# Performance work log

Hardware: AMD Instinct MI355X
Metric: run time of the kernel (lower is better)

The kernel has to match this reference:

```python
import jax, jax.numpy as jnp
import numpy as np
from functools import partial

HID = 16
EMB = 32

def setup_inputs() -> dict:
    key = jax.random.key(0)
    ks = jax.random.split(key, 9)
    S, B, V = 64, 32, 50257
    stdv = 1.0 / np.sqrt(HID)
    u = lambda k, shp: jax.random.uniform(k, shp, jnp.float32, -stdv, stdv)
    return {
        "input_batch": jax.random.randint(ks[0], (S, B), 0, V),
        "embedding": u(ks[1], (V, EMB)),  # original re-inits randn embedding with uniform via init_params
        "W_lr": u(ks[2], (HID, EMB + HID)),
        "b_lr": u(ks[3], (HID,)),
        "W_rl": u(ks[4], (HID, EMB + HID)),
        "b_rl": u(ks[5], (HID,)),
        "W_ho": u(ks[6], (V, 2 * HID)),
        "b_ho": u(ks[7], (V,)),
        "h0": u(ks[8], (1, HID)),
    }


def _rnn_pre_states(emb, W, b, h0):
    # emb: [S,B,E]; returns stacked hidden states BEFORE each step: [S,B,H]
    def step(h, x):
        h_new = jnp.tanh(jnp.concatenate([x, h], axis=-1) @ W.T + b)
        return h_new, h  # collect pre-update state
    _, pre = jax.lax.scan(step, h0, emb)
    return pre


def reference(input_batch, embedding, W_lr, b_lr, W_rl, b_rl, W_ho, b_ho, h0):
    S, B = input_batch.shape
    emb = embedding[input_batch]                      # [S,B,EMB]
    h0b = jnp.broadcast_to(h0, (B, HID))
    # Left-to-right: prediction at i uses hLR state before consuming word i
    hLR_pre = _rnn_pre_states(emb, W_lr, b_lr, h0b)   # [S,B,HID]
    # Right-to-left: run over reversed sequence, collect pre-states, reverse back
    hRL_pre = _rnn_pre_states(emb[::-1], W_rl, b_rl, h0b)[::-1]  # [S,B,HID]
    h = jnp.concatenate([hLR_pre, hRL_pre], axis=-1)  # [S,B,2*HID]
    logits = jnp.einsum('sbh,vh->sbv', h, W_ho) + b_ho
    return jax.nn.log_softmax(logits, axis=-1)        # [S,B,V]
```

## Files before the change

kernel.cpp:

```cpp
#include <hip/hip_runtime.h>
#include <hip/hip_bf16.h>

#define S 64
#define B 32
#define HID 16
#define EMB 32
#define V 50257
#define NCB 197
#define VP4 51200
#define M 2048
#define PREP_BLOCKS (VP4*EMB/256)
#define NRG 4
#define RT_PER (128/NRG)
#define CPG 25

using bf16x8 = __attribute__((ext_vector_type(8))) __bf16;
using f32x4  = __attribute__((ext_vector_type(4))) float;

__global__ void k_prep(const float* __restrict__ W_ho, const float* __restrict__ b_ho,
                       const int* __restrict__ idx, const float* __restrict__ emb,
                       const float* __restrict__ W_lr, const float* __restrict__ b_lr,
                       const float* __restrict__ W_rl, const float* __restrict__ b_rl,
                       __bf16* __restrict__ Wb, float* __restrict__ bias,
                       float* __restrict__ P) {
    const int bx = blockIdx.x;
    if (bx < PREP_BLOCKS) {
        int i = bx * 256 + threadIdx.x;
        if (i < VP4) bias[i] = (i < V) ? b_ho[i] : -1e30f;
        int v = i >> 5;
        Wb[i] = (v < V) ? (__bf16)W_ho[i] : (__bf16)0.f;
    } else {
        int i = (bx - PREP_BLOCKS) * 256 + threadIdx.x;
        const int dir = i >> 15, r = i & 32767, m = r >> 4, j = r & 15;
        const float* W  = dir ? W_rl : W_lr;
        const float* bb = dir ? b_rl : b_lr;
        const int tok = idx[m];
        const float4* er = reinterpret_cast<const float4*>(emb + (size_t)tok * EMB);
        const float4* wr = reinterpret_cast<const float4*>(W + j * (EMB + HID));
        float acc = bb[j];
        #pragma unroll
        for (int q = 0; q < 8; ++q) {
            float4 e4 = er[q], w4 = wr[q];
            acc += e4.x * w4.x + e4.y * w4.y + e4.z * w4.z + e4.w * w4.w;
        }
        P[i] = acc;
    }
}

__global__ void k_rnn(const float* __restrict__ P,
                      const float* __restrict__ W_lr, const float* __restrict__ W_rl,
                      const float* __restrict__ h0, __bf16* __restrict__ hcat) {
    __shared__ float Psh[S * 4 * HID];
    __shared__ float hsh[4][17];
    const int t = threadIdx.x;
    const int dir = blockIdx.x >> 3, bq = blockIdx.x & 7;
    const int bl = t >> 4, j = t & 15;
    const int b = bq * 4 + bl;
    {
        const float4* Pg4 = reinterpret_cast<const float4*>(P);
        float4* Ps4 = reinterpret_cast<float4*>(Psh);
        #pragma unroll
        for (int i = 0; i < 16; ++i) {
            int s = (t >> 4) + 4 * i;
            Ps4[t + 64 * i] = Pg4[dir * 8192 + s * 128 + bq * 16 + (t & 15)];
        }
    }
    const float* Wd = (dir ? W_rl : W_lr) + j * (EMB + HID) + EMB;
    float wh[16];
    #pragma unroll
    for (int q = 0; q < 4; ++q) {
        float4 w4 = *reinterpret_cast<const float4*>(Wd + q * 4);
        wh[q * 4 + 0] = w4.x; wh[q * 4 + 1] = w4.y;
        wh[q * 4 + 2] = w4.z; wh[q * 4 + 3] = w4.w;
    }
    float hcur = h0[j];
    hsh[bl][j] = hcur;
    for (int step = 0; step < S; ++step) {
        const int s = dir ? (S - 1 - step) : step;
        hcat[(s * B + b) * 32 + dir * HID + j] = (__bf16)hcur;
        float acc = Psh[s * 64 + bl * 16 + j];
        #pragma unroll
        for (int k = 0; k < HID; ++k) acc += wh[k] * hsh[bl][k];
        hcur = tanhf(acc);
        hsh[bl][j] = hcur;
    }
}

__global__ void k_pass1(const __bf16* __restrict__ hb, const __bf16* __restrict__ Wb,
                        const float* __restrict__ bias, float* __restrict__ partials) {
    const int cbx = blockIdx.x, rg = blockIdx.y;
    const int wave = threadIdx.x >> 6, lane = threadIdx.x & 63;
    const int lr = lane & 15, kg = lane >> 4;
    const int ttbase = cbx * 16 + wave * 4;
    bf16x8 wfrag[4]; float bc[4];
    #pragma unroll
    for (int q = 0; q < 4; ++q) {
        wfrag[q] = *reinterpret_cast<const bf16x8*>(Wb + ((ttbase + q) * 16 + lr) * 32 + kg * 8);
        bc[q] = bias[(ttbase + q) * 16 + lr];
    }
    __shared__ float red[4][16];
    const f32x4 zero = {0.f, 0.f, 0.f, 0.f};
    for (int rt = rg * RT_PER; rt < rg * RT_PER + RT_PER; ++rt) {
        const int m0 = rt * 16;
        const bf16x8 a = *reinterpret_cast<const bf16x8*>(hb + (m0 + lr) * 32 + kg * 8);
        float s0 = 0.f, s1 = 0.f, s2 = 0.f, s3 = 0.f;
        #pragma unroll
        for (int q = 0; q < 4; ++q) {
            f32x4 d = __builtin_amdgcn_mfma_f32_16x16x32_bf16(a, wfrag[q], zero, 0, 0, 0);
            s0 += __expf(d[0] + bc[q]);
            s1 += __expf(d[1] + bc[q]);
            s2 += __expf(d[2] + bc[q]);
            s3 += __expf(d[3] + bc[q]);
        }
        #pragma unroll
        for (int off = 1; off < 16; off <<= 1) {
            s0 += __shfl_xor(s0, off);
            s1 += __shfl_xor(s1, off);
            s2 += __shfl_xor(s2, off);
            s3 += __shfl_xor(s3, off);
        }
        if (lr == 0) {
            red[wave][kg * 4 + 0] = s0;
            red[wave][kg * 4 + 1] = s1;
            red[wave][kg * 4 + 2] = s2;
            red[wave][kg * 4 + 3] = s3;
        }
        __syncthreads();
        if (threadIdx.x < 16)
            partials[cbx * M + m0 + threadIdx.x] =
                red[0][threadIdx.x] + red[1][threadIdx.x] +
                red[2][threadIdx.x] + red[3][threadIdx.x];
        __syncthreads();
    }
}

__device__ __forceinline__ void p2_load(const __bf16* __restrict__ Wb,
                                        const float* __restrict__ bias,
                                        int chunk, int wave, int lr, int kg,
                                        bf16x8* wf, float* bc) {
    const int t0 = chunk * 16 + wave * 4;
    #pragma unroll
    for (int q = 0; q < 4; ++q) {
        wf[q] = *reinterpret_cast<const bf16x8*>(Wb + ((t0 + q) * 16 + lr) * 32 + kg * 8);
        bc[q] = bias[(t0 + q) * 16 + lr];
    }
}

template <bool GUARD>
__device__ __forceinline__ void p2_cs(const bf16x8* wf, const float* bc, bf16x8 a,
                                      const float* lzr, int chunk, int wave,
                                      int lane, int lr, int kg, int m0,
                                      float* __restrict__ out, float (*st)[68]) {
    const f32x4 zero = {0.f, 0.f, 0.f, 0.f};
    #pragma unroll
    for (int q = 0; q < 4; ++q) {
        f32x4 d = __builtin_amdgcn_mfma_f32_16x16x32_bf16(a, wf[q], zero, 0, 0, 0);
        const int cl = q * 16 + lr;
        #pragma unroll
        for (int r = 0; r < 4; ++r)
            st[kg * 4 + r][cl] = d[r] + bc[q] - lzr[r];
    }
    asm volatile("s_waitcnt lgkmcnt(0)" ::: "memory");
    __builtin_amdgcn_sched_barrier(0);
    const int cb0 = chunk * 256 + wave * 64;
    const int vcol = cb0 + lane;
    float* p = out + (size_t)m0 * V + vcol;
    #pragma unroll
    for (int r = 0; r < 16; ++r) {
        if (!GUARD || vcol < V)
            p[(size_t)r * V] = st[r][lane];
    }
}

__global__ __launch_bounds__(256, 4) void k_pass2(
        const __bf16* __restrict__ hb, const __bf16* __restrict__ Wb,
        const float* __restrict__ bias, const float* __restrict__ partials,
        float* __restrict__ out) {
    __shared__ float red[16][17];
    __shared__ float lzsh[16];
    __shared__ float stg[2][4][16][68];
    const int cg = blockIdx.x, rt = blockIdx.y;
    const int t = threadIdx.x;
    const int m0 = rt * 16;
    {
        const int row = t & 15, cch = t >> 4;
        float p = 0.f;
        for (int c = cch; c < NCB; c += 16) p += partials[c * M + m0 + row];
        red[cch][row] = p;
        __syncthreads();
        if (t < 16) {
            float tot = 0.f;
            #pragma unroll
            for (int k = 0; k < 16; ++k) tot += red[k][t];
            lzsh[t] = __logf(tot);
        }
        __syncthreads();
    }
    const int wave = t >> 6, lane = t & 63;
    const int lr = lane & 15, kg = lane >> 4;
    const bf16x8 a = *reinterpret_cast<const bf16x8*>(hb + (m0 + lr) * 32 + kg * 8);
    float lzr[4];
    #pragma unroll
    for (int r = 0; r < 4; ++r) lzr[r] = lzsh[kg * 4 + r];
    float (*stA)[68] = stg[0][wave];
    float (*stB)[68] = stg[1][wave];
    const int c0 = cg * CPG;

    bf16x8 wfA[4], wfB[4];
    float bcA[4], bcB[4];
    p2_load(Wb, bias, c0, wave, lr, kg, wfA, bcA);
    if (cg < 7) {
        for (int g = 0; g < 12; ++g) {
            p2_load(Wb, bias, c0 + 2 * g + 1, wave, lr, kg, wfB, bcB);
            p2_cs<false>(wfA, bcA, a, lzr, c0 + 2 * g, wave, lane, lr, kg, m0, out, stA);
            p2_load(Wb, bias, c0 + 2 * g + 2, wave, lr, kg, wfA, bcA);
            p2_cs<false>(wfB, bcB, a, lzr, c0 + 2 * g + 1, wave, lane, lr, kg, m0, out, stB);
        }
        p2_cs<false>(wfA, bcA, a, lzr, c0 + 24, wave, lane, lr, kg, m0, out, stA);
    } else {
        for (int g = 0; g < 12; ++g) {
            p2_load(Wb, bias, c0 + 2 * g + 1, wave, lr, kg, wfB, bcB);
            p2_cs<true>(wfA, bcA, a, lzr, c0 + 2 * g, wave, lane, lr, kg, m0, out, stA);
            p2_load(Wb, bias, c0 + 2 * g + 2, wave, lr, kg, wfA, bcA);
            p2_cs<true>(wfB, bcB, a, lzr, c0 + 2 * g + 1, wave, lane, lr, kg, m0, out, stB);
        }
        p2_cs<true>(wfA, bcA, a, lzr, c0 + 24, wave, lane, lr, kg, m0, out, stA);
    }
}

extern "C" void kernel_launch(void* const* d_in, const int* in_sizes, int n_in,
                              void* d_out, int out_size, void* d_ws, size_t ws_size,
                              hipStream_t stream) {
    const int*   idx       = (const int*)d_in[0];
    const float* embedding = (const float*)d_in[1];
    const float* W_lr      = (const float*)d_in[2];
    const float* b_lr      = (const float*)d_in[3];
    const float* W_rl      = (const float*)d_in[4];
    const float* b_rl      = (const float*)d_in[5];
    const float* W_ho      = (const float*)d_in[6];
    const float* b_ho      = (const float*)d_in[7];
    const float* h0        = (const float*)d_in[8];
    float* out = (float*)d_out;

    char* ws = (char*)d_ws;
    size_t off = 0;
    __bf16* Wb      = (__bf16*)(ws + off); off += (size_t)VP4 * EMB * 2;
    float*  bias    = (float*)(ws + off);  off += (size_t)VP4 * 4;
    __bf16* hb      = (__bf16*)(ws + off); off += (size_t)M * 32 * 2;
    float*  P       = (float*)(ws + off);  off += (size_t)2 * M * HID * 4;
    float*  partials= (float*)(ws + off);  off += (size_t)NCB * M * 4;

    k_prep<<<PREP_BLOCKS + 256, 256, 0, stream>>>(W_ho, b_ho, idx, embedding,
                                                  W_lr, b_lr, W_rl, b_rl, Wb, bias, P);
    k_rnn<<<16, 64, 0, stream>>>(P, W_lr, W_rl, h0, hb);
    k_pass1<<<dim3(NCB, NRG), 256, 0, stream>>>(hb, Wb, bias, partials);
    k_pass2<<<dim3(8, 128), 256, 0, stream>>>(hb, Wb, bias, partials, out);
}
```

Measured before the change: 186.2 us.

## Fuse all stages into one cooperative persistent kernel with grid syncs

Replaces the four separate launches (prep, RNN, pass1 partial sums, pass2 write) with a single cooperative kernel of 512 blocks that uses grid-wide syncs between phases. The bf16 weight conversion now runs in parallel with the serial RNN on the otherwise idle blocks, and the logsumexp partials are reduced over 8 column groups instead of 197. Each block handles two row tiles. This removes launch gaps and hides the RNN latency, at the cost of three grid barriers, lower occupancy (launch bounds 2) and a longer serial per-block loop in pass1.

After: 445.4 us. 139% more time.

```diff
diff --git a/kernel.cpp b/kernel.cpp
--- a/kernel.cpp
+++ b/kernel.cpp
@@ -1,36 +1,85 @@
 #include <hip/hip_runtime.h>
 #include <hip/hip_bf16.h>
+#include <hip/hip_cooperative_groups.h>
 
 #define S 64
 #define B 32
 #define HID 16
 #define EMB 32
 #define V 50257
-#define NCB 197
 #define VP4 51200
 #define M 2048
-#define PREP_BLOCKS (VP4*EMB/256)
-#define NRG 4
-#define RT_PER (128/NRG)
+#define NCG 8
+#define TPW 100
 #define CPG 25
+#define WB_STRIDE (496*256)
+
+namespace cgrp = cooperative_groups;
 
 using bf16x8 = __attribute__((ext_vector_type(8))) __bf16;
 using f32x4  = __attribute__((ext_vector_type(4))) float;
 
-__global__ void k_prep(const float* __restrict__ W_ho, const float* __restrict__ b_ho,
-                       const int* __restrict__ idx, const float* __restrict__ emb,
-                       const float* __restrict__ W_lr, const float* __restrict__ b_lr,
-                       const float* __restrict__ W_rl, const float* __restrict__ b_rl,
-                       __bf16* __restrict__ Wb, float* __restrict__ bias,
-                       float* __restrict__ P) {
-    const int bx = blockIdx.x;
-    if (bx < PREP_BLOCKS) {
-        int i = bx * 256 + threadIdx.x;
-        if (i < VP4) bias[i] = (i < V) ? b_ho[i] : -1e30f;
-        int v = i >> 5;
-        Wb[i] = (v < V) ? (__bf16)W_ho[i] : (__bf16)0.f;
-    } else {
-        int i = (bx - PREP_BLOCKS) * 256 + threadIdx.x;
+__device__ __forceinline__ void p2_load(const __bf16* __restrict__ Wb,
+                                        const float* __restrict__ bias,
+                                        int chunk, int wave, int lr, int kg,
+                                        bf16x8* wf, float* bc) {
+    const int t0 = chunk * 16 + wave * 4;
+    #pragma unroll
+    for (int q = 0; q < 4; ++q) {
+        wf[q] = *reinterpret_cast<const bf16x8*>(Wb + ((t0 + q) * 16 + lr) * 32 + kg * 8);
+        bc[q] = bias[(t0 + q) * 16 + lr];
+    }
+}
+
+template <bool GUARD>
+__device__ __forceinline__ void p2_cs(const bf16x8* wf, const float* bc, bf16x8 a,
+                                      const float* lzr, int chunk, int wave,
+                                      int lane, int lr, int kg, int m0,
+                                      float* __restrict__ out, float (*st)[68]) {
+    const f32x4 zero = {0.f, 0.f, 0.f, 0.f};
+    #pragma unroll
+    for (int q = 0; q < 4; ++q) {
+        f32x4 d = __builtin_amdgcn_mfma_f32_16x16x32_bf16(a, wf[q], zero, 0, 0, 0);
+        const int cl = q * 16 + lr;
+        #pragma unroll
+        for (int r = 0; r < 4; ++r)
+            st[kg * 4 + r][cl] = d[r] + bc[q] - lzr[r];
+    }
+    asm volatile("s_waitcnt lgkmcnt(0)" ::: "memory");
+    __builtin_amdgcn_sched_barrier(0);
+    const int cb0 = chunk * 256 + wave * 64;
+    const int vcol = cb0 + lane;
+    float* p = out + (size_t)m0 * V + vcol;
+    #pragma unroll
+    for (int r = 0; r < 16; ++r) {
+        if (!GUARD || vcol < V)
+            p[(size_t)r * V] = st[r][lane];
+    }
+}
+
+__global__ __launch_bounds__(256, 2) void k_all(
+        const int* __restrict__ idx, const float* __restrict__ emb,
+        const float* __restrict__ W_lr, const float* __restrict__ b_lr,
+        const float* __restrict__ W_rl, const float* __restrict__ b_rl,
+        const float* __restrict__ W_ho, const float* __restrict__ b_ho,
+        const float* __restrict__ h0,
+        __bf16* __restrict__ Wb, float* __restrict__ bias,
+        __bf16* __restrict__ hb, float* __restrict__ P,
+        float* __restrict__ Zp, float* __restrict__ out) {
+    __shared__ float Psh[S * 4 * HID];
+    __shared__ float hsh[4][17];
+    __shared__ float red[2][4][16];
+    __shared__ float lzsh[2][16];
+    __shared__ float stg[2][4][16][68];
+
+    const int cg = blockIdx.x, ry = blockIdx.y;
+    const int bid = cg + NCG * ry;
+    const int t = threadIdx.x;
+    const int gtid = bid * 256 + t;
+
+    if (gtid < VP4) bias[gtid] = (gtid < V) ? b_ho[gtid] : -1e30f;
+    if (gtid < 2 * M * HID) {
+        const int i = gtid;
         const int dir = i >> 15, r = i & 32767, m = r >> 4, j = r & 15;
         const float* W  = dir ? W_rl : W_lr;
         const float* bb = dir ? b_rl : b_lr;
@@ -45,186 +94,125 @@
         }
         P[i] = acc;
     }
-}
-
-__global__ void k_rnn(const float* __restrict__ P,
-                      const float* __restrict__ W_lr, const float* __restrict__ W_rl,
-                      const float* __restrict__ h0, __bf16* __restrict__ hcat) {
-    __shared__ float Psh[S * 4 * HID];
-    __shared__ float hsh[4][17];
-    const int t = threadIdx.x;
-    const int dir = blockIdx.x >> 3, bq = blockIdx.x & 7;
-    const int bl = t >> 4, j = t & 15;
-    const int b = bq * 4 + bl;
-    {
-        const float4* Pg4 = reinterpret_cast<const float4*>(P);
-        float4* Ps4 = reinterpret_cast<float4*>(Psh);
-        #pragma unroll
-        for (int i = 0; i < 16; ++i) {
-            int s = (t >> 4) + 4 * i;
-            Ps4[t + 64 * i] = Pg4[dir * 8192 + s * 128 + bq * 16 + (t & 15)];
-        }
-    }
-    const float* Wd = (dir ? W_rl : W_lr) + j * (EMB + HID) + EMB;
-    float wh[16];
-    #pragma unroll
-    for (int q = 0; q < 4; ++q) {
-        float4 w4 = *reinterpret_cast<const float4*>(Wd + q * 4);
-        wh[q * 4 + 0] = w4.x; wh[q * 4 + 1] = w4.y;
-        wh[q * 4 + 2] = w4.z; wh[q * 4 + 3] = w4.w;
-    }
-    float hcur = h0[j];
-    hsh[bl][j] = hcur;
-    for (int step = 0; step < S; ++step) {
-        const int s = dir ? (S - 1 - step) : step;
-        hcat[(s * B + b) * 32 + dir * HID + j] = (__bf16)hcur;
-        float acc = Psh[s * 64 + bl * 16 + j];
-        #pragma unroll
-        for (int k = 0; k < HID; ++k) acc += wh[k] * hsh[bl][k];
-        hcur = tanhf(acc);
-        hsh[bl][j] = hcur;
-    }
-}
-
-__global__ void k_pass1(const __bf16* __restrict__ hb, const __bf16* __restrict__ Wb,
-                        const float* __restrict__ bias, float* __restrict__ partials) {
-    const int cbx = blockIdx.x, rg = blockIdx.y;
-    const int wave = threadIdx.x >> 6, lane = threadIdx.x & 63;
-    const int lr = lane & 15, kg = lane >> 4;
-    const int ttbase = cbx * 16 + wave * 4;
-    bf16x8 wfrag[4]; float bc[4];
-    #pragma unroll
-    for (int q = 0; q < 4; ++q) {
-        wfrag[q] = *reinterpret_cast<const bf16x8*>(Wb + ((ttbase + q) * 16 + lr) * 32 + kg * 8);
-        bc[q] = bias[(ttbase + q) * 16 + lr];
-    }
-    __shared__ float red[4][16];
-    const f32x4 zero = {0.f, 0.f, 0.f, 0.f};
-    for (int rt = rg * RT_PER; rt < rg * RT_PER + RT_PER; ++rt) {
-        const int m0 = rt * 16;
-        const bf16x8 a = *reinterpret_cast<const bf16x8*>(hb + (m0 + lr) * 32 + kg * 8);
-        float s0 = 0.f, s1 = 0.f, s2 = 0.f, s3 = 0.f;
-        #pragma unroll
-        for (int q = 0; q < 4; ++q) {
-            f32x4 d = __builtin_amdgcn_mfma_f32_16x16x32_bf16(a, wfrag[q], zero, 0, 0, 0);
-            s0 += __expf(d[0] + bc[q]);
-            s1 += __expf(d[1] + bc[q]);
-            s2 += __expf(d[2] + bc[q]);
-            s3 += __expf(d[3] + bc[q]);
-        }
-        #pragma unroll
-        for (int off = 1; off < 16; off <<= 1) {
-            s0 += __shfl_xor(s0, off);
-            s1 += __shfl_xor(s1, off);
-            s2 += __shfl_xor(s2, off);
-            s3 += __shfl_xor(s3, off);
-        }
-        if (lr == 0) {
-            red[wave][kg * 4 + 0] = s0;
-            red[wave][kg * 4 + 1] = s1;
-            red[wave][kg * 4 + 2] = s2;
-            red[wave][kg * 4 + 3] = s3;
-        }
-        __syncthreads();
-        if (threadIdx.x < 16)
-            partials[cbx * M + m0 + threadIdx.x] =
-                red[0][threadIdx.x] + red[1][threadIdx.x] +
-                red[2][threadIdx.x] + red[3][threadIdx.x];
-        __syncthreads();
-    }
-}
-
-__device__ __forceinline__ void p2_load(const __bf16* __restrict__ Wb,
-                                        const float* __restrict__ bias,
-                                        int chunk, int wave, int lr, int kg,
-                                        bf16x8* wf, float* bc) {
-    const int t0 = chunk * 16 + wave * 4;
-    #pragma unroll
-    for (int q = 0; q < 4; ++q) {
-        wf[q] = *reinterpret_cast<const bf16x8*>(Wb + ((t0 + q) * 16 + lr) * 32 + kg * 8);
-        bc[q] = bias[(t0 + q) * 16 + lr];
-    }
-}
-
-template <bool GUARD>
-__device__ __forceinline__ void p2_cs(const bf16x8* wf, const float* bc, bf16x8 a,
-                                      const float* lzr, int chunk, int wave,
-                                      int lane, int lr, int kg, int m0,
-                                      float* __restrict__ out, float (*st)[68]) {
-    const f32x4 zero = {0.f, 0.f, 0.f, 0.f};
-    #pragma unroll
-    for (int q = 0; q < 4; ++q) {
-        f32x4 d = __builtin_amdgcn_mfma_f32_16x16x32_bf16(a, wf[q], zero, 0, 0, 0);
-        const int cl = q * 16 + lr;
-        #pragma unroll
-        for (int r = 0; r < 4; ++r)
-            st[kg * 4 + r][cl] = d[r] + bc[q] - lzr[r];
-    }
-    asm volatile("s_waitcnt lgkmcnt(0)" ::: "memory");
-    __builtin_amdgcn_sched_barrier(0);
-    const int cb0 = chunk * 256 + wave * 64;
-    const int vcol = cb0 + lane;
-    float* p = out + (size_t)m0 * V + vcol;
-    #pragma unroll
-    for (int r = 0; r < 16; ++r) {
-        if (!GUARD || vcol < V)
-            p[(size_t)r * V] = st[r][lane];
-    }
-}
-
-__global__ __launch_bounds__(256, 4) void k_pass2(
-        const __bf16* __restrict__ hb, const __bf16* __restrict__ Wb,
-        const float* __restrict__ bias, const float* __restrict__ partials,
-        float* __restrict__ out) {
-    __shared__ float red[16][17];
-    __shared__ float lzsh[16];
-    __shared__ float stg[2][4][16][68];
-    const int cg = blockIdx.x, rt = blockIdx.y;
-    const int t = threadIdx.x;
-    const int m0 = rt * 16;
-    {
-        const int row = t & 15, cch = t >> 4;
-        float p = 0.f;
-        for (int c = cch; c < NCB; c += 16) p += partials[c * M + m0 + row];
-        red[cch][row] = p;
-        __syncthreads();
-        if (t < 16) {
-            float tot = 0.f;
+    __threadfence();
+    cgrp::this_grid().sync();
+
+    if (bid < 16) {
+        if (t < 64) {
+            const int dir = bid >> 3, bq = bid & 7;
+            const int bl = t >> 4, j = t & 15;
+            const int b = bq * 4 + bl;
+            {
+                const float4* Pg4 = reinterpret_cast<const float4*>(P);
+                float4* Ps4 = reinterpret_cast<float4*>(Psh);
+                #pragma unroll
+                for (int i = 0; i < 16; ++i) {
+                    int s = (t >> 4) + 4 * i;
+                    Ps4[t + 64 * i] = Pg4[dir * 8192 + s * 128 + bq * 16 + (t & 15)];
+                }
+            }
+            const float* Wd = (dir ? W_rl : W_lr) + j * (EMB + HID) + EMB;
+            float wh[16];
             #pragma unroll
-            for (int k = 0; k < 16; ++k) tot += red[k][t];
-            lzsh[t] = __logf(tot);
-        }
-        __syncthreads();
-    }
+            for (int q = 0; q < 4; ++q) {
+                float4 w4 = *reinterpret_cast<const float4*>(Wd + q * 4);
+                wh[q * 4 + 0] = w4.x; wh[q * 4 + 1] = w4.y;
+                wh[q * 4 + 2] = w4.z; wh[q * 4 + 3] = w4.w;
+            }
+            float hcur = h0[j];
+            hsh[bl][j] = hcur;
+            for (int step = 0; step < S; ++step) {
+                const int s = dir ? (S - 1 - step) : step;
+                hb[(s * B + b) * 32 + dir * HID + j] = (__bf16)hcur;
+                float acc = Psh[s * 64 + bl * 16 + j];
+                #pragma unroll
+                for (int k = 0; k < HID; ++k) acc += wh[k] * hsh[bl][k];
+                hcur = tanhf(acc);
+                hsh[bl][j] = hcur;
+            }
+        }
+    } else {
+        for (int i = (bid - 16) * 256 + t; i < VP4 * EMB; i += WB_STRIDE) {
+            int v = i >> 5;
+            Wb[i] = (v < V) ? (__bf16)W_ho[i] : (__bf16)0.f;
+        }
+    }
+    __threadfence();
+    cgrp::this_grid().sync();
+
     const int wave = t >> 6, lane = t & 63;
     const int lr = lane & 15, kg = lane >> 4;
-    const bf16x8 a = *reinterpret_cast<const bf16x8*>(hb + (m0 + lr) * 32 + kg * 8);
-    float lzr[4];
-    #pragma unroll
-    for (int r = 0; r < 4; ++r) lzr[r] = lzsh[kg * 4 + r];
+    const int rt0 = ry * 2;
+    const int tb = cg * 400 + wave * TPW;
+    const f32x4 zero = {0.f, 0.f, 0.f, 0.f};
+    #pragma unroll
+    for (int h = 0; h < 2; ++h) {
+        const int m0 = (rt0 + h) * 16;
+        const bf16x8 a = *reinterpret_cast<const bf16x8*>(hb + (m0 + lr) * 32 + kg * 8);
+        float s = 0.f;
+        for (int tt = tb; tt < tb + TPW; ++tt) {
+            bf16x8 wf = *reinterpret_cast<const bf16x8*>(Wb + (tt * 16 + lr) * 32 + kg * 8);
+            f32x4 b4 = *reinterpret_cast<const f32x4*>(bias + tt * 16 + kg * 4);
+            f32x4 d = __builtin_amdgcn_mfma_f32_16x16x32_bf16(wf, a, zero, 0, 0, 0);
+            s += __expf(d[0] + b4[0]) + __expf(d[1] + b4[1]) +
+                 __expf(d[2] + b4[2]) + __expf(d[3] + b4[3]);
+        }
+        s += __shfl_xor(s, 16);
+        s += __shfl_xor(s, 32);
+        if (lane < 16) red[h][wave][lane] = s;
+    }
+    __syncthreads();
+    if (t < 32) {
+        const int h = t >> 4, row = t & 15;
+        float z = red[h][0][row] + red[h][1][row] + red[h][2][row] + red[h][3][row];
+        __hip_atomic_store(&Zp[cg * M + (rt0 + h) * 16 + row], z,
+                           __ATOMIC_RELAXED, __HIP_MEMORY_SCOPE_AGENT);
+    }
+    __threadfence();
+    cgrp::this_grid().sync();
+
+    if (t < 32) {
+        const int h = t >> 4, row = t & 15;
+        float z = 0.f;
+        #pragma unroll
+        for (int c = 0; c < NCG; ++c)
+            z += __hip_atomic_load(&Zp[c * M + (rt0 + h) * 16 + row],
+                                   __ATOMIC_RELAXED, __HIP_MEMORY_SCOPE_AGENT);
+        lzsh[h][row] = __logf(z);
+    }
+    __syncthreads();
+
     float (*stA)[68] = stg[0][wave];
     float (*stB)[68] = stg[1][wave];
     const int c0 = cg * CPG;
-
-    bf16x8 wfA[4], wfB[4];
-    float bcA[4], bcB[4];
-    p2_load(Wb, bias, c0, wave, lr, kg, wfA, bcA);
-    if (cg < 7) {
-        for (int g = 0; g < 12; ++g) {
-            p2_load(Wb, bias, c0 + 2 * g + 1, wave, lr, kg, wfB, bcB);
-            p2_cs<false>(wfA, bcA, a, lzr, c0 + 2 * g, wave, lane, lr, kg, m0, out, stA);
-            p2_load(Wb, bias, c0 + 2 * g + 2, wave, lr, kg, wfA, bcA);
-            p2_cs<false>(wfB, bcB, a, lzr, c0 + 2 * g + 1, wave, lane, lr, kg, m0, out, stB);
-        }
-        p2_cs<false>(wfA, bcA, a, lzr, c0 + 24, wave, lane, lr, kg, m0, out, stA);
-    } else {
-        for (int g = 0; g < 12; ++g) {
-            p2_load(Wb, bias, c0 + 2 * g + 1, wave, lr, kg, wfB, bcB);
-            p2_cs<true>(wfA, bcA, a, lzr, c0 + 2 * g, wave, lane, lr, kg, m0, out, stA);
-            p2_load(Wb, bias, c0 + 2 * g + 2, wave, lr, kg, wfA, bcA);
-            p2_cs<true>(wfB, bcB, a, lzr, c0 + 2 * g + 1, wave, lane, lr, kg, m0, out, stB);
-        }
-        p2_cs<true>(wfA, bcA, a, lzr, c0 + 24, wave, lane, lr, kg, m0, out, stA);
+    #pragma unroll
+    for (int h = 0; h < 2; ++h) {
+        const int m0 = (rt0 + h) * 16;
+        const bf16x8 a = *reinterpret_cast<const bf16x8*>(hb + (m0 + lr) * 32 + kg * 8);
+        float lzr[4];
+        #pragma unroll
+        for (int r = 0; r < 4; ++r) lzr[r] = lzsh[h][kg * 4 + r];
+
+        bf16x8 wfA[4], wfB[4];
+        float bcA[4], bcB[4];
+        p2_load(Wb, bias, c0, wave, lr, kg, wfA, bcA);
+        if (cg < 7) {
+            for (int g = 0; g < 12; ++g) {
+                p2_load(Wb, bias, c0 + 2 * g + 1, wave, lr, kg, wfB, bcB);
+                p2_cs<false>(wfA, bcA, a, lzr, c0 + 2 * g, wave, lane, lr, kg, m0, out, stA);
+                p2_load(Wb, bias, c0 + 2 * g + 2, wave, lr, kg, wfA, bcA);
+                p2_cs<false>(wfB, bcB, a, lzr, c0 + 2 * g + 1, wave, lane, lr, kg, m0, out, stB);
+            }
+            p2_cs<false>(wfA, bcA, a, lzr, c0 + 24, wave, lane, lr, kg, m0, out, stA);
+        } else {
+            for (int g = 0; g < 12; ++g) {
+                p2_load(Wb, bias, c0 + 2 * g + 1, wave, lr, kg, wfB, bcB);
+                p2_cs<true>(wfA, bcA, a, lzr, c0 + 2 * g, wave, lane, lr, kg, m0, out, stA);
+                p2_load(Wb, bias, c0 + 2 * g + 2, wave, lr, kg, wfA, bcA);
+                p2_cs<true>(wfB, bcB, a, lzr, c0 + 2 * g + 1, wave, lane, lr, kg, m0, out, stB);
+            }
+            p2_cs<true>(wfA, bcA, a, lzr, c0 + 24, wave, lane, lr, kg, m0, out, stA);
+        }
     }
 }
 
@@ -244,15 +232,17 @@
 
     char* ws = (char*)d_ws;
     size_t off = 0;
-    __bf16* Wb      = (__bf16*)(ws + off); off += (size_t)VP4 * EMB * 2;
-    float*  bias    = (float*)(ws + off);  off += (size_t)VP4 * 4;
-    __bf16* hb      = (__bf16*)(ws + off); off += (size_t)M * 32 * 2;
-    float*  P       = (float*)(ws + off);  off += (size_t)2 * M * HID * 4;
-    float*  partials= (float*)(ws + off);  off += (size_t)NCB * M * 4;
-
-    k_prep<<<PREP_BLOCKS + 256, 256, 0, stream>>>(W_ho, b_ho, idx, embedding,
-                                                  W_lr, b_lr, W_rl, b_rl, Wb, bias, P);
-    k_rnn<<<16, 64, 0, stream>>>(P, W_lr, W_rl, h0, hb);
-    k_pass1<<<dim3(NCB, NRG), 256, 0, stream>>>(hb, Wb, bias, partials);
-    k_pass2<<<dim3(8, 128), 256, 0, stream>>>(hb, Wb, bias, partials, out);
-}
+    __bf16* Wb   = (__bf16*)(ws + off); off += (size_t)VP4 * EMB * 2;
+    float*  bias = (float*)(ws + off);  off += (size_t)VP4 * 4;
+    __bf16* hb   = (__bf16*)(ws + off); off += (size_t)M * 32 * 2;
+    float*  P    = (float*)(ws + off);  off += (size_t)2 * M * HID * 4;
+    float*  Zp   = (float*)(ws + off);  off += (size_t)NCG * M * 4;
+
+    void* kargs[] = { (void*)&idx, (void*)&embedding,
+                      (void*)&W_lr, (void*)&b_lr, (void*)&W_rl, (void*)&b_rl,
+                      (void*)&W_ho, (void*)&b_ho, (void*)&h0,
+                      (void*)&Wb, (void*)&bias, (void*)&hb, (void*)&P,
+                      (void*)&Zp, (void*)&out };
+    hipLaunchCooperativeKernel((const void*)k_all, dim3(NCG, 64), dim3(256),
+                               kargs, 0, stream);
+}
```
